# Performance work log

Measured on AMD Instinct MI355X. Metric: run time of the kernel, lower is better.

## Reference

```python
import jax, jax.numpy as jnp
import numpy as np

NEG = -1e8


def lstm_scan(x, lens, Wih, Whh, b):
    # x: [B,S,D], lens: [B] int. PyTorch gate order i,f,g,o. Returns [B,S,H], zero at pad.
    B, S, D = x.shape
    H = Whh.shape[1]
    xs = jnp.swapaxes(x, 0, 1)  # [S,B,D]
    ts = jnp.arange(S)

    def step(carry, inp):
        h, c = carry
        xt, t = inp
        gates = xt @ Wih.T + h @ Whh.T + b  # [B,4H]
        i, f, g, o = jnp.split(gates, 4, axis=-1)
        i, f, o = jax.nn.sigmoid(i), jax.nn.sigmoid(f), jax.nn.sigmoid(o)
        g = jnp.tanh(g)
        c_new = f * c + i * g
        h_new = o * jnp.tanh(c_new)
        valid = (t < lens)[:, None]
        h = jnp.where(valid, h_new, h)
        c = jnp.where(valid, c_new, c)
        out = jnp.where(valid, h_new, 0.0)
        return (h, c), out

    init = (jnp.zeros((B, H), x.dtype), jnp.zeros((B, H), x.dtype))
    _, outs = jax.lax.scan(step, init, (xs, ts))
    return jnp.swapaxes(outs, 0, 1)  # [B,S,H]


def bilstm(x, lens, Wih_f, Whh_f, b_f, Wih_b, Whh_b, b_b):
    # forward direction
    out_f = lstm_scan(x, lens, Wih_f, Whh_f, b_f)
    # backward: reverse the valid prefix per sample (packed-sequence semantics)
    S = x.shape[1]
    t = jnp.arange(S)[None, :]
    idx = jnp.where(t < lens[:, None], lens[:, None] - 1 - t, t)  # [B,S]
    xr = jnp.take_along_axis(x, idx[:, :, None], axis=1)
    out_r = lstm_scan(xr, lens, Wih_b, Whh_b, b_b)
    out_b = jnp.take_along_axis(out_r, idx[:, :, None], axis=1)
    return jnp.concatenate([out_f, out_b], axis=-1)


def tnet_forward(seqs_id, seqs_len, asps_len, asps_mask, sent_mask,
                 embed, Wih_f, Whh_f, b_f, Wih_b, Whh_b, b_b,
                 W_cpt, b_cpt, W_as, b_as, Wq, bq, Wk, bk, Wv, bv, Wd, bd):
    seqs = embed[seqs_id]                                   # [B,S,D] (dropout = eval identity)
    seqs_lstm = bilstm(seqs, seqs_len, Wih_f, Whh_f, b_f, Wih_b, Whh_b, b_b)  # [B,S,D]

    # ragged aspect gather + pad + mean == masked mean (asps_mask==0 marks aspect tokens)
    asp_sel = (asps_mask == 0).astype(seqs_lstm.dtype)       # [B,S]
    asps = (seqs_lstm * asp_sel[:, :, None]).sum(axis=1) / asps_len[:, None].astype(seqs_lstm.dtype)
    asps = asps[:, None, :]                                  # [B,1,D]

    # CPT layers (flag='AS'); Attentions = dot-product attn, out = softmax(QK^T + mask) @ K
    x = seqs_lstm
    for _ in range(2):
        score = jax.nn.softmax(jnp.einsum('bqd,bkd->bqk', x, seqs_lstm) + asps_mask[:, None, :], axis=-1)
        attn_out = jnp.einsum('bqk,bkd->bqd', score, seqs_lstm)
        combine = jnp.concatenate([attn_out, x], axis=-1)    # [B,S,2D]
        linear_out = jax.nn.relu(combine @ W_cpt.T + b_cpt)
        scale = jax.nn.sigmoid(x @ W_as.T + b_as)
        x = scale * linear_out + (1.0 - scale) * x

    # QKVAttention over sentence
    D = x.shape[-1]
    Qp = asps @ Wq.T + bq                                    # [B,1,D]
    Kp = x @ Wk.T + bk                                       # [B,S,D]
    Vp = x @ Wv.T + bv
    sc = jax.nn.softmax(jnp.einsum('bqd,bkd->bqk', Qp, Kp) / jnp.sqrt(jnp.asarray(D, x.dtype))
                        + sent_mask[:, None, :], axis=-1)    # [B,1,S]
    out = jnp.einsum('bqk,bkd->bqd', sc, Vp)                 # [B,1,D]
    logits = out[:, 0] @ Wd.T + bd                           # [B,n_class]
    return logits, sc[:, 0]


def setup_inputs() -> dict:
    B, S, V, D, H, NC = 64, 256, 30000, 512, 256, 3
    key = jax.random.key(0)
    ks = jax.random.split(key, 24)

    seqs_id = jax.random.randint(ks[0], (B, S), 0, V)
    seqs_len = jax.random.randint(ks[1], (B,), S // 2, S + 1)
    asps_len = jax.random.randint(ks[2], (B,), 1, 6)
    start = jax.random.randint(ks[3], (B,), 0, S // 2 - 8)   # aspect span inside valid prefix
    pos = jnp.arange(S)[None, :]
    in_span = (pos >= start[:, None]) & (pos < (start + asps_len)[:, None])
    asps_mask = jnp.where(in_span, 0.0, NEG).astype(jnp.float32)
    sent_mask = jnp.where(pos < seqs_len[:, None], 0.0, NEG).astype(jnp.float32)

    def nrm(k, shape, s=0.02):
        return (s * jax.random.normal(k, shape)).astype(jnp.float32)

    inp = dict(seqs_id=seqs_id, seqs_len=seqs_len, asps_len=asps_len,
               asps_mask=asps_mask, sent_mask=sent_mask,
               embed=nrm(ks[4], (V, D), 0.1),
               Wih_f=nrm(ks[5], (4 * H, D)), Whh_f=nrm(ks[6], (4 * H, H)), b_f=jnp.zeros((4 * H,), jnp.float32),
               Wih_b=nrm(ks[7], (4 * H, D)), Whh_b=nrm(ks[8], (4 * H, H)), b_b=jnp.zeros((4 * H,), jnp.float32),
               W_cpt=nrm(ks[9], (D, 2 * D)), b_cpt=jnp.zeros((D,), jnp.float32),
               W_as=nrm(ks[10], (D, D)), b_as=jnp.zeros((D,), jnp.float32),
               Wq=nrm(ks[11], (D, D)), bq=jnp.zeros((D,), jnp.float32),
               Wk=nrm(ks[12], (D, D)), bk=jnp.zeros((D,), jnp.float32),
               Wv=nrm(ks[13], (D, D)), bv=jnp.zeros((D,), jnp.float32),
               Wd=nrm(ks[14], (NC, D)), bd=jnp.zeros((NC,), jnp.float32))
    return inp


def reference(seqs_id, seqs_len, asps_len, asps_mask, sent_mask,
              embed, Wih_f, Whh_f, b_f, Wih_b, Whh_b, b_b,
              W_cpt, b_cpt, W_as, b_as, Wq, bq, Wk, bk, Wv, bv, Wd, bd):
    return tnet_forward(seqs_id, seqs_len, asps_len, asps_mask, sent_mask,
                        embed, Wih_f, Whh_f, b_f, Wih_b, Whh_b, b_b,
                        W_cpt, b_cpt, W_as, b_as, Wq, bq, Wk, bk, Wv, bv, Wd, bd)
```

## Files before the change

### kernel.cpp

```cpp
#include <hip/hip_runtime.h>
#include <math.h>

constexpr int B_ = 64, S_ = 256, D_ = 512, H_ = 256, NC_ = 3;
constexpr int BS = B_ * S_;
constexpr int G4 = 4 * H_;

typedef __attribute__((ext_vector_type(4))) float f32x4;
typedef __attribute__((ext_vector_type(8))) short s16x8;
typedef unsigned short u16;
typedef unsigned long long u64;

template<int ACT>
static __device__ __forceinline__ float activate(float v) {
  if constexpr (ACT == 1) return v > 0.f ? v : 0.f;
  else if constexpr (ACT == 2) return 1.f / (1.f + expf(-v));
  else return v;
}

static __device__ __forceinline__ u16 f2bf_rne(float f) {
  unsigned u = __float_as_uint(f);
  return (u16)((u + 0x7FFFu + ((u >> 16) & 1u)) >> 16);
}
static __device__ __forceinline__ float bf2f(u16 h) {
  return __uint_as_float(((unsigned)h) << 16);
}
static __device__ __forceinline__ void splitf(float f, u16& h, u16& l) {
  h = f2bf_rne(f);
  float r = f - bf2f(h);
  l = f2bf_rne(r);
}

__global__ __launch_bounds__(256) void split_w(
    const float* __restrict__ src, u16* __restrict__ h, u16* __restrict__ l, int n4)
{
  int i = blockIdx.x * 256 + threadIdx.x;
  if (i >= n4) return;
  float4 v = ((const float4*)src)[i];
  ushort4 hh, ll;
  splitf(v.x, hh.x, ll.x); splitf(v.y, hh.y, ll.y);
  splitf(v.z, hh.z, ll.z); splitf(v.w, hh.w, ll.w);
  ((ushort4*)h)[i] = hh;
  ((ushort4*)l)[i] = ll;
}

__global__ __launch_bounds__(256) void gather_split(
    const float* __restrict__ embed, const int* __restrict__ gidx,
    u16* __restrict__ h, u16* __restrict__ l)
{
  int i = blockIdx.x * 256 + threadIdx.x;
  if (i >= BS * D_ / 4) return;
  int r = i >> 7;
  int c = (i & 127) << 2;
  float4 v = *(const float4*)(embed + (size_t)gidx[r] * D_ + c);
  ushort4 hh, ll;
  splitf(v.x, hh.x, ll.x); splitf(v.y, hh.y, ll.y);
  splitf(v.z, hh.z, ll.z); splitf(v.w, hh.w, ll.w);
  ((ushort4*)h)[i] = hh;
  ((ushort4*)l)[i] = ll;
}

template<int ACT, bool BT, bool ADDC, bool ASPL, bool BSPL, bool OSPL, bool A2>
__global__ __launch_bounds__(256) void mgemm(
    const float* __restrict__ Af, const u16* __restrict__ Ah, const u16* __restrict__ Al,
    const u16* __restrict__ Ah2, const u16* __restrict__ Al2,
    const float* __restrict__ Bf, const u16* __restrict__ Bh, const u16* __restrict__ Bl,
    const float* __restrict__ bias, const float* __restrict__ Cin,
    float* __restrict__ Co, u16* __restrict__ Oh, u16* __restrict__ Ol,
    int M, int N, int K, int ldb, long sA, long sB, long sC, int ksp)
{
  __shared__ u16 AH[128][40];
  __shared__ u16 AL[128][40];
  __shared__ u16 BH[128][40];
  __shared__ u16 BL[128][40];

  const int tid = threadIdx.x;
  const int w = tid >> 6, l = tid & 63;
  const int m0 = blockIdx.x * 128, n0 = blockIdx.y * 128;
  const long zA = (long)blockIdx.z * sA;
  const long zB = (long)blockIdx.z * sB;
  const long zC = (long)blockIdx.z * sC;

  f32x4 acc[2][8];
  #pragma unroll
  for (int i = 0; i < 2; ++i)
    #pragma unroll
    for (int j = 0; j < 8; ++j) acc[i][j] = (f32x4){0.f, 0.f, 0.f, 0.f};

  const int ar = tid >> 1, ahh = tid & 1;
  const int bk = tid >> 3, bnq = tid & 7;
  const int lr = l & 15, lk = (l >> 4) * 8;

  for (int kt = 0; kt < K; kt += 32) {
    {
      int m = m0 + ar;
      if constexpr (ASPL) {
        const u16* srcH = Ah;
        const u16* srcL = Al;
        int kc = kt, kspan = K;
        if constexpr (A2) {
          if (kt >= ksp) { srcH = Ah2; srcL = Al2; kc = kt - ksp; }
          kspan = ksp;
        }
        s16x8 h0 = (s16x8)0, h1 = (s16x8)0, l0 = (s16x8)0, l1 = (s16x8)0;
        if (m < M) {
          const u16* ph = srcH + zA + (size_t)m * kspan + kc + ahh * 16;
          const u16* pl = srcL + zA + (size_t)m * kspan + kc + ahh * 16;
          h0 = *(const s16x8*)ph; h1 = *(const s16x8*)(ph + 8);
          l0 = *(const s16x8*)pl; l1 = *(const s16x8*)(pl + 8);
        }
        *(s16x8*)&AH[ar][ahh * 16] = h0; *(s16x8*)&AH[ar][ahh * 16 + 8] = h1;
        *(s16x8*)&AL[ar][ahh * 16] = l0; *(s16x8*)&AL[ar][ahh * 16 + 8] = l1;
      } else {
        float vv[16];
        if (m < M) {
          const float* pf = Af + zA + (size_t)m * K + kt + ahh * 16;
          #pragma unroll
          for (int c = 0; c < 4; ++c) {
            float4 v = ((const float4*)pf)[c];
            vv[c * 4] = v.x; vv[c * 4 + 1] = v.y; vv[c * 4 + 2] = v.z; vv[c * 4 + 3] = v.w;
          }
        } else {
          #pragma unroll
          for (int c = 0; c < 16; ++c) vv[c] = 0.f;
        }
        u16 hh[16], ll[16];
        #pragma unroll
        for (int c = 0; c < 16; ++c) splitf(vv[c], hh[c], ll[c]);
        *(s16x8*)&AH[ar][ahh * 16] = *(s16x8*)&hh[0];
        *(s16x8*)&AH[ar][ahh * 16 + 8] = *(s16x8*)&hh[8];
        *(s16x8*)&AL[ar][ahh * 16] = *(s16x8*)&ll[0];
        *(s16x8*)&AL[ar][ahh * 16 + 8] = *(s16x8*)&ll[8];
      }
    }
    if constexpr (BT) {
      if constexpr (BSPL) {
        const u16* ph = Bh + zB + (size_t)(n0 + ar) * ldb + kt + ahh * 16;
        const u16* pl = Bl + zB + (size_t)(n0 + ar) * ldb + kt + ahh * 16;
        *(s16x8*)&BH[ar][ahh * 16] = *(const s16x8*)ph;
        *(s16x8*)&BH[ar][ahh * 16 + 8] = *(const s16x8*)(ph + 8);
        *(s16x8*)&BL[ar][ahh * 16] = *(const s16x8*)pl;
        *(s16x8*)&BL[ar][ahh * 16 + 8] = *(const s16x8*)(pl + 8);
      } else {
        const float* pf = Bf + zB + (size_t)(n0 + ar) * ldb + kt + ahh * 16;
        float vv[16];
        #pragma unroll
        for (int c = 0; c < 4; ++c) {
          float4 v = ((const float4*)pf)[c];
          vv[c * 4] = v.x; vv[c * 4 + 1] = v.y; vv[c * 4 + 2] = v.z; vv[c * 4 + 3] = v.w;
        }
        u16 hh[16], ll[16];
        #pragma unroll
        for (int c = 0; c < 16; ++c) splitf(vv[c], hh[c], ll[c]);
        *(s16x8*)&BH[ar][ahh * 16] = *(s16x8*)&hh[0];
        *(s16x8*)&BH[ar][ahh * 16 + 8] = *(s16x8*)&hh[8];
        *(s16x8*)&BL[ar][ahh * 16] = *(s16x8*)&ll[0];
        *(s16x8*)&BL[ar][ahh * 16 + 8] = *(s16x8*)&ll[8];
      }
    } else {
      const u16* ph = Bh + zB + (size_t)(kt + bk) * ldb + n0 + bnq * 16;
      const u16* pl = Bl + zB + (size_t)(kt + bk) * ldb + n0 + bnq * 16;
      s16x8 h8a = *(const s16x8*)ph, h8b = *(const s16x8*)(ph + 8);
      s16x8 l8a = *(const s16x8*)pl, l8b = *(const s16x8*)(pl + 8);
      #pragma unroll
      for (int jj = 0; jj < 8; ++jj) {
        BH[bnq * 16 + jj][bk] = (u16)h8a[jj];
        BH[bnq * 16 + 8 + jj][bk] = (u16)h8b[jj];
        BL[bnq * 16 + jj][bk] = (u16)l8a[jj];
        BL[bnq * 16 + 8 + jj][bk] = (u16)l8b[jj];
      }
    }
    __syncthreads();

    s16x8 afh[2], afl[2];
    #pragma unroll
    for (int i = 0; i < 2; ++i) {
      afh[i] = *(const s16x8*)&AH[w * 32 + i * 16 + lr][lk];
      afl[i] = *(const s16x8*)&AL[w * 32 + i * 16 + lr][lk];
    }
    #pragma unroll
    for (int j = 0; j < 8; ++j) {
      s16x8 bfh = *(const s16x8*)&BH[j * 16 + lr][lk];
      s16x8 bfl = *(const s16x8*)&BL[j * 16 + lr][lk];
      #pragma unroll
      for (int i = 0; i < 2; ++i) {
        acc[i][j] = __builtin_amdgcn_mfma_f32_16x16x32_bf16(afl[i], bfh, acc[i][j], 0, 0, 0);
        acc[i][j] = __builtin_amdgcn_mfma_f32_16x16x32_bf16(afh[i], bfl, acc[i][j], 0, 0, 0);
        acc[i][j] = __builtin_amdgcn_mfma_f32_16x16x32_bf16(afh[i], bfh, acc[i][j], 0, 0, 0);
      }
    }
    __syncthreads();
  }

  const int rl = (l >> 4) * 4;
  #pragma unroll
  for (int j = 0; j < 8; ++j) {
    int n = n0 + j * 16 + lr;
    float bv = bias ? bias[n] : 0.f;
    #pragma unroll
    for (int i = 0; i < 2; ++i) {
      #pragma unroll
      for (int e = 0; e < 4; ++e) {
        int m = m0 + w * 32 + i * 16 + rl + e;
        if (m < M) {
          float v = acc[i][j][e] + bv;
          if constexpr (ADDC) v += Cin[zC + (size_t)m * N + n];
          v = activate<ACT>(v);
          if constexpr (OSPL) {
            u16 hh, ll; splitf(v, hh, ll);
            Oh[zC + (size_t)m * N + n] = hh;
            Ol[zC + (size_t)m * N + n] = ll;
          } else {
            Co[zC + (size_t)m * N + n] = v;
          }
        }
      }
    }
  }
}

__global__ __launch_bounds__(256) void wf_prep(
    const float* __restrict__ Wf, const float* __restrict__ Wb, u16* __restrict__ WF)
{
  int gid = blockIdx.x * 256 + threadIdx.x;
  int lane = gid & 63;
  int nt = (gid >> 6) & 1;
  int kt = (gid >> 7) & 7;
  int w  = (gid >> 10) & 3;
  int j  = (gid >> 12) & 7;
  int dir = gid >> 15;
  const float* W = dir ? Wb : Wf;
  int r = w * 256 + j * 32 + nt * 16 + (lane & 15);
  int kb = kt * 32 + (lane >> 4) * 8;
  const float* src = W + (size_t)r * H_ + kb;
  u16 hh[8], ll[8];
  #pragma unroll
  for (int c = 0; c < 2; ++c) {
    float4 v = ((const float4*)src)[c];
    splitf(v.x, hh[c*4+0], ll[c*4+0]); splitf(v.y, hh[c*4+1], ll[c*4+1]);
    splitf(v.z, hh[c*4+2], ll[c*4+2]); splitf(v.w, hh[c*4+3], ll[c*4+3]);
  }
  size_t off = (size_t)(gid >> 6) * 1024 + (size_t)lane * 8;
  *(s16x8*)(WF + off)       = *(s16x8*)&hh[0];
  *(s16x8*)(WF + off + 512) = *(s16x8*)&ll[0];
}

__global__ __launch_bounds__(256) void ring_init(u64* __restrict__ ring64)
{
  int i = blockIdx.x * 256 + threadIdx.x;
  __hip_atomic_store(&ring64[i], (u64)3, __ATOMIC_RELAXED, __HIP_MEMORY_SCOPE_AGENT);
}

__global__ __launch_bounds__(256, 1) void lstm_dist(
    const float* __restrict__ GX, const u16* __restrict__ WF,
    const int* __restrict__ lens, u16* __restrict__ outH, u16* __restrict__ outL,
    u64* __restrict__ ring64)
{
  const int bid = blockIdx.x;
  const int grp = bid & 7;
  const int j   = bid >> 3;
  const int dir = grp >> 2;
  const int bg  = grp & 3;
  const int b0g = bg * 16;
  const int tid = threadIdx.x;
  const int w = tid >> 6, l = tid & 63;

  const float* gx = GX + (size_t)dir * ((size_t)BS * G4);

  __shared__ int slen[16];
  __shared__ __align__(16) u16 AHs[16][264];
  __shared__ __align__(16) u16 ALs[16][264];
  __shared__ float act[2][4][16][33];
  if (tid < 16) slen[tid] = lens[b0g + tid];
  __syncthreads();

  s16x8 wh[8][2], wl[8][2];
  #pragma unroll
  for (int kt = 0; kt < 8; ++kt)
    #pragma unroll
    for (int nt = 0; nt < 2; ++nt) {
      size_t q = ((size_t)(((dir * 8 + j) * 4 + w) * 8 + kt) * 2 + nt);
      const u16* p = WF + q * 1024 + (size_t)l * 8;
      wh[kt][nt] = *(const s16x8*)p;
      wl[kt][nt] = *(const s16x8*)(p + 512);
    }

  const int ub = tid >> 4;
  const int uu = (tid & 15) * 2;
  const int len_b = slen[ub];
  float c0s = 0.f, c1s = 0.f, h0s = 0.f, h1s = 0.f;

  const int lr = l & 15, lkb = (l >> 4) * 8;

  for (int t = 0; t < S_; ++t) {
    float gxv[2][4];
    #pragma unroll
    for (int nt = 0; nt < 2; ++nt)
      #pragma unroll
      for (int e = 0; e < 4; ++e) {
        int b = (l >> 4) * 4 + e;
        int len = slen[b];
        int pos = dir ? (t < len ? len - 1 - t : t) : t;
        gxv[nt][e] = gx[(size_t)((b0g + b) * S_ + pos) * G4 + (w * 256 + j * 32 + nt * 16 + lr)];
      }

    f32x4 acc[2];
    acc[0] = (f32x4){0.f, 0.f, 0.f, 0.f};
    acc[1] = (f32x4){0.f, 0.f, 0.f, 0.f};

    if (t > 0) {
      const unsigned gen = (unsigned)(((t - 1) >> 2) & 3);
      const int slot = (t - 1) & 3;
      u64* rb = ring64 + ((size_t)slot * 8 + grp) * (16 * 128);
      u64 v[8];
      unsigned need = 0xFFu;
      do {
        unsigned nn = 0;
        #pragma unroll
        for (int k = 0; k < 8; ++k)
          if ((need >> k) & 1)
            v[k] = __hip_atomic_load(&rb[k * 256 + tid], __ATOMIC_RELAXED, __HIP_MEMORY_SCOPE_AGENT);
        #pragma unroll
        for (int k = 0; k < 8; ++k)
          if (((need >> k) & 1) && ((unsigned)v[k] & 3u) != gen) nn |= 1u << k;
        need = nn;
      } while (need);
      #pragma unroll
      for (int k = 0; k < 8; ++k) {
        int idx = k * 256 + tid;
        int b = idx >> 7, p = idx & 127;
        float f0 = __uint_as_float((unsigned)v[k] & ~3u);
        float f1 = __uint_as_float((unsigned)(v[k] >> 32));
        u16 hh0, ll0, hh1, ll1;
        splitf(f0, hh0, ll0); splitf(f1, hh1, ll1);
        *(unsigned*)&AHs[b][2 * p] = (unsigned)hh0 | ((unsigned)hh1 << 16);
        *(unsigned*)&ALs[b][2 * p] = (unsigned)ll0 | ((unsigned)ll1 << 16);
      }
      __syncthreads();
      #pragma unroll
      for (int kt = 0; kt < 8; ++kt) {
        s16x8 ah = *(const s16x8*)&AHs[lr][kt * 32 + lkb];
        s16x8 al = *(const s16x8*)&ALs[lr][kt * 32 + lkb];
        #pragma unroll
        for (int nt = 0; nt < 2; ++nt) {
          acc[nt] = __builtin_amdgcn_mfma_f32_16x16x32_bf16(al, wh[kt][nt], acc[nt], 0, 0, 0);
          acc[nt] = __builtin_amdgcn_mfma_f32_16x16x32_bf16(ah, wl[kt][nt], acc[nt], 0, 0, 0);
          acc[nt] = __builtin_amdgcn_mfma_f32_16x16x32_bf16(ah, wh[kt][nt], acc[nt], 0, 0, 0);
        }
      }
    }

    const int pb = t & 1;
    #pragma unroll
    for (int nt = 0; nt < 2; ++nt)
      #pragma unroll
      for (int e = 0; e < 4; ++e) {
        float v = acc[nt][e] + gxv[nt][e];
        v = (w == 2) ? tanhf(v) : 1.f / (1.f + expf(-v));
        act[pb][w][(l >> 4) * 4 + e][nt * 16 + lr] = v;
      }
    __syncthreads();

    {
      int pos = dir ? (t < len_b ? len_b - 1 - t : t) : t;
      bool valid = t < len_b;
      float i0 = act[pb][0][ub][uu],     f0 = act[pb][1][ub][uu],     g0 = act[pb][2][ub][uu],     o0 = act[pb][3][ub][uu];
      float i1 = act[pb][0][ub][uu + 1], f1 = act[pb][1][ub][uu + 1], g1 = act[pb][2][ub][uu + 1], o1 = act[pb][3][ub][uu + 1];
      float cn0 = fmaf(f0, c0s, i0 * g0), cn1 = fmaf(f1, c1s, i1 * g1);
      float hn0 = o0 * tanhf(cn0), hn1 = o1 * tanhf(cn1);
      if (valid) { c0s = cn0; h0s = hn0; c1s = cn1; h1s = hn1; }
      unsigned gen = (unsigned)((t >> 2) & 3);
      unsigned a0 = (__float_as_uint(h0s) & ~3u) | gen;
      unsigned a1 = __float_as_uint(h1s);
      u64 word = ((u64)a1 << 32) | (u64)a0;
      const int slot = t & 3;
      size_t ridx = ((size_t)slot * 8 + grp) * (16 * 128) + (size_t)ub * 128 + j * 16 + (tid & 15);
      __hip_atomic_store(&ring64[ridx], word, __ATOMIC_RELAXED, __HIP_MEMORY_SCOPE_AGENT);
      float ov0 = valid ? hn0 : 0.f, ov1 = valid ? hn1 : 0.f;
      u16 oh0, qq0, oh1, qq1;
      splitf(ov0, oh0, qq0); splitf(ov1, oh1, qq1);
      size_t obase = (size_t)((b0g + ub) * S_ + pos) * (2 * H_) + dir * H_ + j * 32 + uu;
      *(ushort2*)&outH[obase] = make_ushort2(oh0, oh1);
      *(ushort2*)&outL[obase] = make_ushort2(qq0, qq1);
    }
  }
}

__global__ __launch_bounds__(512) void asps_k(
    const u16* __restrict__ lh, const u16* __restrict__ ll,
    const float* __restrict__ amask, const int* __restrict__ alen, float* __restrict__ asps)
{
  int b = blockIdx.x, tid = threadIdx.x;
  __shared__ int sstart;
  if (tid == 0) sstart = S_;
  __syncthreads();
  if (tid < S_ && amask[b * S_ + tid] == 0.f) atomicMin(&sstart, tid);
  __syncthreads();
  const int start = sstart;
  const int len = alen[b];
  float acc = 0.f;
  for (int k = 0; k < len; ++k) {
    size_t i = ((size_t)(b * S_ + start + k)) * D_ + tid;
    acc += bf2f(lh[i]) + bf2f(ll[i]);
  }
  asps[b * D_ + tid] = acc / (float)len;
}

__global__ __launch_bounds__(256) void softmax_rows(
    const float* __restrict__ p_, const float* __restrict__ mask,
    u16* __restrict__ ph, u16* __restrict__ pl)
{
  const int row = blockIdx.x;
  const int b = row >> 8;
  const int tid = threadIdx.x;
  const float* p = p_ + (size_t)row * S_;
  float v = p[tid] + mask[(b << 8) | tid];
  float m = v;
  #pragma unroll
  for (int off = 32; off > 0; off >>= 1) m = fmaxf(m, __shfl_xor(m, off));
  __shared__ float r1[4];
  __shared__ float r2[4];
  const int w = tid >> 6, l = tid & 63;
  if (l == 0) r1[w] = m;
  __syncthreads();
  m = fmaxf(fmaxf(r1[0], r1[1]), fmaxf(r1[2], r1[3]));
  float e = expf(v - m);
  float s = e;
  #pragma unroll
  for (int off = 32; off > 0; off >>= 1) s += __shfl_xor(s, off);
  if (l == 0) r2[w] = s;
  __syncthreads();
  s = r2[0] + r2[1] + r2[2] + r2[3];
  float o = e / s;
  u16 hh, ll; splitf(o, hh, ll);
  ph[(size_t)row * S_ + tid] = hh;
  pl[(size_t)row * S_ + tid] = ll;
}

__global__ __launch_bounds__(256) void xupdate(
    const u16* __restrict__ xh, const u16* __restrict__ xl,
    const float4* __restrict__ sc, const float4* __restrict__ lin,
    u16* __restrict__ oh, u16* __restrict__ ol, int n4)
{
  int i = blockIdx.x * 256 + threadIdx.x;
  if (i >= n4) return;
  ushort4 h4 = ((const ushort4*)xh)[i];
  ushort4 l4 = ((const ushort4*)xl)[i];
  float4 s = sc[i], lv = lin[i];
  float x0 = bf2f(h4.x) + bf2f(l4.x);
  float x1 = bf2f(h4.y) + bf2f(l4.y);
  float x2 = bf2f(h4.z) + bf2f(l4.z);
  float x3 = bf2f(h4.w) + bf2f(l4.w);
  float o0 = s.x * lv.x + (1.f - s.x) * x0;
  float o1 = s.y * lv.y + (1.f - s.y) * x1;
  float o2 = s.z * lv.z + (1.f - s.z) * x2;
  float o3 = s.w * lv.w + (1.f - s.w) * x3;
  ushort4 hh, ll;
  splitf(o0, hh.x, ll.x); splitf(o1, hh.y, ll.y);
  splitf(o2, hh.z, ll.z); splitf(o3, hh.w, ll.w);
  ((ushort4*)oh)[i] = hh;
  ((ushort4*)ol)[i] = ll;
}

__global__ __launch_bounds__(256) void final_sc_k(
    const float* __restrict__ Qp, const float* __restrict__ Kp,
    const float* __restrict__ smask, float* __restrict__ outsc)
{
  int b = blockIdx.x, tid = threadIdx.x;
  __shared__ float q[D_];
  q[tid] = Qp[b * D_ + tid];
  q[tid + 256] = Qp[b * D_ + tid + 256];
  __syncthreads();
  const float4* kr = (const float4*)(Kp + ((size_t)(b * S_ + tid)) * D_);
  float acc = 0.f;
  #pragma unroll 4
  for (int d = 0; d < D_ / 4; ++d) {
    float4 kv = kr[d];
    acc += q[4 * d] * kv.x + q[4 * d + 1] * kv.y + q[4 * d + 2] * kv.z + q[4 * d + 3] * kv.w;
  }
  float v = acc / sqrtf((float)D_) + smask[b * S_ + tid];
  float m = v;
  #pragma unroll
  for (int off = 32; off > 0; off >>= 1) m = fmaxf(m, __shfl_xor(m, off));
  __shared__ float r1[4];
  __shared__ float r2[4];
  const int w = tid >> 6, l = tid & 63;
  if (l == 0) r1[w] = m;
  __syncthreads();
  m = fmaxf(fmaxf(r1[0], r1[1]), fmaxf(r1[2], r1[3]));
  float e = expf(v - m);
  float s = e;
  #pragma unroll
  for (int off = 32; off > 0; off >>= 1) s += __shfl_xor(s, off);
  if (l == 0) r2[w] = s;
  __syncthreads();
  s = r2[0] + r2[1] + r2[2] + r2[3];
  outsc[b * S_ + tid] = e / s;
}

__global__ __launch_bounds__(512) void zero_outv(float* __restrict__ p)
{
  p[blockIdx.x * 512 + threadIdx.x] = 0.f;
}

__global__ __launch_bounds__(512) void out_vec_k(
    const float* __restrict__ sc, const float* __restrict__ Vp, float* __restrict__ outv)
{
  int b = blockIdx.x, d = threadIdx.x;
  int k0 = blockIdx.y * 32;
  __shared__ float s[32];
  if (d < 32) s[d] = sc[b * S_ + k0 + d];
  __syncthreads();
  float acc = 0.f;
  #pragma unroll
  for (int k = 0; k < 32; ++k)
    acc = fmaf(s[k], Vp[((size_t)(b * S_ + k0 + k)) * D_ + d], acc);
  atomicAdd(&outv[b * D_ + d], acc);
}

__global__ __launch_bounds__(192) void logits_k(
    const float* __restrict__ outv, const float* __restrict__ Wd,
    const float* __restrict__ bd, float* __restrict__ out)
{
  int b = blockIdx.x;
  int c = threadIdx.x >> 6, l = threadIdx.x & 63;
  float acc = 0.f;
  for (int d = l; d < D_; d += 64) acc = fmaf(outv[b * D_ + d], Wd[c * D_ + d], acc);
  #pragma unroll
  for (int off = 32; off > 0; off >>= 1) acc += __shfl_down(acc, off);
  if (l == 0) out[b * NC_ + c] = acc + bd[c];
}

extern "C" void kernel_launch(void* const* d_in, const int* in_sizes, int n_in,
                              void* d_out, int out_size, void* d_ws, size_t ws_size,
                              hipStream_t stream)
{
  const int*   seqs_id   = (const int*)d_in[0];
  const int*   seqs_len  = (const int*)d_in[1];
  const int*   asps_len  = (const int*)d_in[2];
  const float* asps_mask = (const float*)d_in[3];
  const float* sent_mask = (const float*)d_in[4];
  const float* embed     = (const float*)d_in[5];
  const float* Wih_f     = (const float*)d_in[6];
  const float* Whh_f     = (const float*)d_in[7];
  const float* b_f       = (const float*)d_in[8];
  const float* Wih_b     = (const float*)d_in[9];
  const float* Whh_b     = (const float*)d_in[10];
  const float* b_b       = (const float*)d_in[11];
  const float* W_cpt     = (const float*)d_in[12];
  const float* b_cpt     = (const float*)d_in[13];
  const float* W_as      = (const float*)d_in[14];
  const float* b_as      = (const float*)d_in[15];
  const float* Wq        = (const float*)d_in[16];
  const float* bq        = (const float*)d_in[17];
  const float* Wk        = (const float*)d_in[18];
  const float* bk        = (const float*)d_in[19];
  const float* Wv        = (const float*)d_in[20];
  const float* bv        = (const float*)d_in[21];
  const float* Wd        = (const float*)d_in[22];
  const float* bd        = (const float*)d_in[23];

  float* w = (float*)d_ws;
  size_t off = 0;
  auto alloc = [&](size_t words) { size_t o = off; off += words; return o; };
  struct Split { u16* h; u16* l; };
  auto salloc = [&](size_t n) {
    size_t o = alloc(n);
    Split s; s.h = (u16*)(w + o); s.l = (u16*)(w + o) + n; return s;
  };

  const size_t off_wf   = alloc(524288);
  const size_t off_ring = alloc(131072);
  Split sWihF = salloc(4ul * H_ * D_);
  Split sWihB = salloc(4ul * H_ * D_);
  Split sWcpt = salloc((size_t)D_ * 2 * D_);
  Split sWas  = salloc((size_t)D_ * D_);
  Split sWk   = salloc((size_t)D_ * D_);
  Split sWv   = salloc((size_t)D_ * D_);
  Split sWq   = salloc((size_t)D_ * D_);
  Split sLstm = salloc((size_t)BS * D_);
  const size_t off_asps = alloc((size_t)B_ * D_);
  const size_t off_qp   = alloc((size_t)B_ * D_);
  const size_t off_outv = alloc((size_t)B_ * D_);

  const size_t dyn0 = off;
  Split sXemb; sXemb.h = (u16*)(w + dyn0); sXemb.l = sXemb.h + (size_t)BS * D_;
  float* GX = w + dyn0 + (size_t)BS * D_;
  size_t p2 = dyn0;
  float* scoreF = w + p2;                 p2 += (size_t)B_ * S_ * S_;
  Split sScore; sScore.h = (u16*)(w + p2); sScore.l = sScore.h + (size_t)B_ * S_ * S_; p2 += (size_t)B_ * S_ * S_;
  Split sAttn;  sAttn.h  = (u16*)(w + p2); sAttn.l  = sAttn.h + (size_t)BS * D_;       p2 += (size_t)BS * D_;
  float* lin = w + p2;                    p2 += (size_t)BS * D_;
  float* scl = w + p2;                    p2 += (size_t)BS * D_;
  Split sX;     sX.h     = (u16*)(w + p2); sX.l     = sX.h + (size_t)BS * D_;           p2 += (size_t)BS * D_;

  u16* WF      = (u16*)(w + off_wf);
  u64* ring64  = (u64*)(w + off_ring);
  float* aspsb = w + off_asps;
  float* qp    = w + off_qp;
  float* outv  = w + off_outv;
  float* Kp    = (float*)sAttn.h;
  float* Vp    = lin;
  float* logits = (float*)d_out;
  float* outsc  = (float*)d_out + B_ * NC_;

  ring_init<<<256, 256, 0, stream>>>(ring64);
  wf_prep<<<256, 256, 0, stream>>>(Whh_f, Whh_b, WF);
  split_w<<<512, 256, 0, stream>>>(Wih_f, sWihF.h, sWihF.l, H_ * D_);
  split_w<<<512, 256, 0, stream>>>(Wih_b, sWihB.h, sWihB.l, H_ * D_);
  split_w<<<512, 256, 0, stream>>>(W_cpt, sWcpt.h, sWcpt.l, D_ * 2 * D_ / 4);
  split_w<<<256, 256, 0, stream>>>(W_as, sWas.h, sWas.l, D_ * D_ / 4);
  split_w<<<256, 256, 0, stream>>>(Wk, sWk.h, sWk.l, D_ * D_ / 4);
  split_w<<<256, 256, 0, stream>>>(Wv, sWv.h, sWv.l, D_ * D_ / 4);
  split_w<<<256, 256, 0, stream>>>(Wq, sWq.h, sWq.l, D_ * D_ / 4);
  gather_split<<<BS * D_ / 4 / 256, 256, 0, stream>>>(embed, seqs_id, sXemb.h, sXemb.l);

  mgemm<0, true, false, true, true, false, false><<<dim3(128, 8, 1), 256, 0, stream>>>(
      nullptr, sXemb.h, sXemb.l, nullptr, nullptr, nullptr, sWihF.h, sWihF.l, b_f, nullptr,
      GX, nullptr, nullptr, BS, G4, D_, D_, 0, 0, 0, 0);
  mgemm<0, true, false, true, true, false, false><<<dim3(128, 8, 1), 256, 0, stream>>>(
      nullptr, sXemb.h, sXemb.l, nullptr, nullptr, nullptr, sWihB.h, sWihB.l, b_b, nullptr,
      GX + (size_t)BS * G4, nullptr, nullptr, BS, G4, D_, D_, 0, 0, 0, 0);

  lstm_dist<<<64, 256, 0, stream>>>(GX, WF, seqs_len, sLstm.h, sLstm.l, ring64);
  asps_k<<<B_, 512, 0, stream>>>(sLstm.h, sLstm.l, asps_mask, asps_len, aspsb);

  for (int it = 0; it < 2; ++it) {
    const Split xin = (it == 0) ? sLstm : sX;
    mgemm<0, true, false, true, true, false, false><<<dim3(2, 2, B_), 256, 0, stream>>>(
        nullptr, xin.h, xin.l, nullptr, nullptr, nullptr, sLstm.h, sLstm.l, nullptr, nullptr,
        scoreF, nullptr, nullptr, S_, S_, D_, D_,
        (long)S_ * D_, (long)S_ * D_, (long)S_ * S_, 0);
    softmax_rows<<<BS, 256, 0, stream>>>(scoreF, asps_mask, sScore.h, sScore.l);
    mgemm<0, false, false, true, true, true, false><<<dim3(2, 4, B_), 256, 0, stream>>>(
        nullptr, sScore.h, sScore.l, nullptr, nullptr, nullptr, sLstm.h, sLstm.l, nullptr, nullptr,
        nullptr, sAttn.h, sAttn.l, S_, D_, S_, D_,
        (long)S_ * S_, (long)S_ * D_, (long)S_ * D_, 0);
    mgemm<1, true, false, true, true, false, true><<<dim3(128, 4, 1), 256, 0, stream>>>(
        nullptr, sAttn.h, sAttn.l, xin.h, xin.l, nullptr, sWcpt.h, sWcpt.l, b_cpt, nullptr,
        lin, nullptr, nullptr, BS, D_, 2 * D_, 2 * D_, 0, 0, 0, D_);
    mgemm<2, true, false, true, true, false, false><<<dim3(128, 4, 1), 256, 0, stream>>>(
        nullptr, xin.h, xin.l, nullptr, nullptr, nullptr, sWas.h, sWas.l, b_as, nullptr,
        scl, nullptr, nullptr, BS, D_, D_, D_, 0, 0, 0, 0);
    xupdate<<<(BS * D_ / 4 + 255) / 256, 256, 0, stream>>>(
        xin.h, xin.l, (const float4*)scl, (const float4*)lin, sX.h, sX.l, BS * D_ / 4);
  }

  mgemm<0, true, false, true, true, false, false><<<dim3(128, 4, 1), 256, 0, stream>>>(
      nullptr, sX.h, sX.l, nullptr, nullptr, nullptr, sWk.h, sWk.l, bk, nullptr,
      Kp, nullptr, nullptr, BS, D_, D_, D_, 0, 0, 0, 0);
  mgemm<0, true, false, true, true, false, false><<<dim3(128, 4, 1), 256, 0, stream>>>(
      nullptr, sX.h, sX.l, nullptr, nullptr, nullptr, sWv.h, sWv.l, bv, nullptr,
      Vp, nullptr, nullptr, BS, D_, D_, D_, 0, 0, 0, 0);
  mgemm<0, true, false, false, true, false, false><<<dim3(1, 4, 1), 256, 0, stream>>>(
      aspsb, nullptr, nullptr, nullptr, nullptr, nullptr, sWq.h, sWq.l, bq, nullptr,
      qp, nullptr, nullptr, B_, D_, D_, D_, 0, 0, 0, 0);

  zero_outv<<<B_ * D_ / 512, 512, 0, stream>>>(outv);
  final_sc_k<<<B_, 256, 0, stream>>>(qp, Kp, sent_mask, outsc);
  out_vec_k<<<dim3(B_, 8, 1), 512, 0, stream>>>(outsc, Vp, outv);
  logits_k<<<B_, 192, 0, stream>>>(outv, Wd, bd, logits);
}
```

Before: 1.518 ms.

## Fuse score GEMM with masked softmax and fold gate update into GEMM epilogue

```diff
diff --git a/kernel.cpp b/kernel.cpp
--- a/kernel.cpp
+++ b/kernel.cpp
@@ -59,7 +59,7 @@
   ((ushort4*)l)[i] = ll;
 }
 
-template<int ACT, bool BT, bool ADDC, bool ASPL, bool BSPL, bool OSPL, bool A2>
+template<int ACT, bool BT, bool ADDC, bool ASPL, bool BSPL, bool OSPL, bool A2, bool XUP>
 __global__ __launch_bounds__(256) void mgemm(
     const float* __restrict__ Af, const u16* __restrict__ Ah, const u16* __restrict__ Al,
     const u16* __restrict__ Ah2, const u16* __restrict__ Al2,
@@ -205,7 +205,14 @@
           float v = acc[i][j][e] + bv;
           if constexpr (ADDC) v += Cin[zC + (size_t)m * N + n];
           v = activate<ACT>(v);
-          if constexpr (OSPL) {
+          if constexpr (XUP) {
+            float lv = Cin[zC + (size_t)m * N + n];
+            float xv = bf2f(Ah2[(size_t)m * N + n]) + bf2f(Al2[(size_t)m * N + n]);
+            float o = v * lv + (1.f - v) * xv;
+            u16 hh, ll; splitf(o, hh, ll);
+            Oh[zC + (size_t)m * N + n] = hh;
+            Ol[zC + (size_t)m * N + n] = ll;
+          } else if constexpr (OSPL) {
             u16 hh, ll; splitf(v, hh, ll);
             Oh[zC + (size_t)m * N + n] = hh;
             Ol[zC + (size_t)m * N + n] = ll;
@@ -213,6 +220,111 @@
             Co[zC + (size_t)m * N + n] = v;
           }
         }
+      }
+    }
+  }
+}
+
+__global__ __launch_bounds__(256) void score_sm(
+    const u16* __restrict__ Ah, const u16* __restrict__ Al,
+    const u16* __restrict__ Bh, const u16* __restrict__ Bl,
+    const float* __restrict__ mask,
+    u16* __restrict__ Oh, u16* __restrict__ Ol)
+{
+  __shared__ u16 AH[128][40];
+  __shared__ u16 AL[128][40];
+  __shared__ u16 BH[256][40];
+  __shared__ u16 BL[256][40];
+
+  const int tid = threadIdx.x;
+  const int w = tid >> 6, l = tid & 63;
+  const int m0 = blockIdx.x * 128;
+  const int z  = blockIdx.y;
+  const long zA = (long)z * (S_ * D_);
+  const long zC = (long)z * (S_ * S_);
+
+  f32x4 acc[2][16];
+  #pragma unroll
+  for (int i = 0; i < 2; ++i)
+    #pragma unroll
+    for (int j = 0; j < 16; ++j) acc[i][j] = (f32x4){0.f, 0.f, 0.f, 0.f};
+
+  const int ar = tid >> 1, ahh = tid & 1;
+  const int lr = l & 15, lk = (l >> 4) * 8;
+
+  for (int kt = 0; kt < D_; kt += 32) {
+    {
+      const u16* ph = Ah + zA + (size_t)(m0 + ar) * D_ + kt + ahh * 16;
+      const u16* pl = Al + zA + (size_t)(m0 + ar) * D_ + kt + ahh * 16;
+      *(s16x8*)&AH[ar][ahh * 16] = *(const s16x8*)ph;
+      *(s16x8*)&AH[ar][ahh * 16 + 8] = *(const s16x8*)(ph + 8);
+      *(s16x8*)&AL[ar][ahh * 16] = *(const s16x8*)pl;
+      *(s16x8*)&AL[ar][ahh * 16 + 8] = *(const s16x8*)(pl + 8);
+    }
+    #pragma unroll
+    for (int h = 0; h < 2; ++h) {
+      int r = h * 128 + ar;
+      const u16* ph = Bh + zA + (size_t)r * D_ + kt + ahh * 16;
+      const u16* pl = Bl + zA + (size_t)r * D_ + kt + ahh * 16;
+      *(s16x8*)&BH[r][ahh * 16] = *(const s16x8*)ph;
+      *(s16x8*)&BH[r][ahh * 16 + 8] = *(const s16x8*)(ph + 8);
+      *(s16x8*)&BL[r][ahh * 16] = *(const s16x8*)pl;
+      *(s16x8*)&BL[r][ahh * 16 + 8] = *(const s16x8*)(pl + 8);
+    }
+    __syncthreads();
+
+    s16x8 afh[2], afl[2];
+    #pragma unroll
+    for (int i = 0; i < 2; ++i) {
+      afh[i] = *(const s16x8*)&AH[w * 32 + i * 16 + lr][lk];
+      afl[i] = *(const s16x8*)&AL[w * 32 + i * 16 + lr][lk];
+    }
+    #pragma unroll
+    for (int j = 0; j < 16; ++j) {
+      s16x8 bfh = *(const s16x8*)&BH[j * 16 + lr][lk];
+      s16x8 bfl = *(const s16x8*)&BL[j * 16 + lr][lk];
+      #pragma unroll
+      for (int i = 0; i < 2; ++i) {
+        acc[i][j] = __builtin_amdgcn_mfma_f32_16x16x32_bf16(afl[i], bfh, acc[i][j], 0, 0, 0);
+        acc[i][j] = __builtin_amdgcn_mfma_f32_16x16x32_bf16(afh[i], bfl, acc[i][j], 0, 0, 0);
+        acc[i][j] = __builtin_amdgcn_mfma_f32_16x16x32_bf16(afh[i], bfh, acc[i][j], 0, 0, 0);
+      }
+    }
+    __syncthreads();
+  }
+
+  const int rl = (l >> 4) * 4;
+  float mk[16];
+  #pragma unroll
+  for (int j = 0; j < 16; ++j) mk[j] = mask[z * S_ + j * 16 + lr];
+
+  #pragma unroll
+  for (int i = 0; i < 2; ++i) {
+    #pragma unroll
+    for (int e = 0; e < 4; ++e) {
+      float val[16];
+      float vmax = -1e30f;
+      #pragma unroll
+      for (int j = 0; j < 16; ++j) {
+        val[j] = acc[i][j][e] + mk[j];
+        vmax = fmaxf(vmax, val[j]);
+      }
+      #pragma unroll
+      for (int off = 1; off < 16; off <<= 1)
+        vmax = fmaxf(vmax, __shfl_xor(vmax, off));
+      float sum = 0.f;
+      #pragma unroll
+      for (int j = 0; j < 16; ++j) { val[j] = expf(val[j] - vmax); sum += val[j]; }
+      #pragma unroll
+      for (int off = 1; off < 16; off <<= 1)
+        sum += __shfl_xor(sum, off);
+      float inv = 1.f / sum;
+      int r = m0 + w * 32 + i * 16 + rl + e;
+      #pragma unroll
+      for (int j = 0; j < 16; ++j) {
+        u16 hh, ll; splitf(val[j] * inv, hh, ll);
+        Oh[zC + (size_t)r * S_ + j * 16 + lr] = hh;
+        Ol[zC + (size_t)r * S_ + j * 16 + lr] = ll;
       }
     }
   }
@@ -403,62 +515,6 @@
     acc += bf2f(lh[i]) + bf2f(ll[i]);
   }
   asps[b * D_ + tid] = acc / (float)len;
-}
-
-__global__ __launch_bounds__(256) void softmax_rows(
-    const float* __restrict__ p_, const float* __restrict__ mask,
-    u16* __restrict__ ph, u16* __restrict__ pl)
-{
-  const int row = blockIdx.x;
-  const int b = row >> 8;
-  const int tid = threadIdx.x;
-  const float* p = p_ + (size_t)row * S_;
-  float v = p[tid] + mask[(b << 8) | tid];
-  float m = v;
-  #pragma unroll
-  for (int off = 32; off > 0; off >>= 1) m = fmaxf(m, __shfl_xor(m, off));
-  __shared__ float r1[4];
-  __shared__ float r2[4];
-  const int w = tid >> 6, l = tid & 63;
-  if (l == 0) r1[w] = m;
-  __syncthreads();
-  m = fmaxf(fmaxf(r1[0], r1[1]), fmaxf(r1[2], r1[3]));
-  float e = expf(v - m);
-  float s = e;
-  #pragma unroll
-  for (int off = 32; off > 0; off >>= 1) s += __shfl_xor(s, off);
-  if (l == 0) r2[w] = s;
-  __syncthreads();
-  s = r2[0] + r2[1] + r2[2] + r2[3];
-  float o = e / s;
-  u16 hh, ll; splitf(o, hh, ll);
-  ph[(size_t)row * S_ + tid] = hh;
-  pl[(size_t)row * S_ + tid] = ll;
-}
-
-__global__ __launch_bounds__(256) void xupdate(
-    const u16* __restrict__ xh, const u16* __restrict__ xl,
-    const float4* __restrict__ sc, const float4* __restrict__ lin,
-    u16* __restrict__ oh, u16* __restrict__ ol, int n4)
-{
-  int i = blockIdx.x * 256 + threadIdx.x;
-  if (i >= n4) return;
-  ushort4 h4 = ((const ushort4*)xh)[i];
-  ushort4 l4 = ((const ushort4*)xl)[i];
-  float4 s = sc[i], lv = lin[i];
-  float x0 = bf2f(h4.x) + bf2f(l4.x);
-  float x1 = bf2f(h4.y) + bf2f(l4.y);
-  float x2 = bf2f(h4.z) + bf2f(l4.z);
-  float x3 = bf2f(h4.w) + bf2f(l4.w);
-  float o0 = s.x * lv.x + (1.f - s.x) * x0;
-  float o1 = s.y * lv.y + (1.f - s.y) * x1;
-  float o2 = s.z * lv.z + (1.f - s.z) * x2;
-  float o3 = s.w * lv.w + (1.f - s.w) * x3;
-  ushort4 hh, ll;
-  splitf(o0, hh.x, ll.x); splitf(o1, hh.y, ll.y);
-  splitf(o2, hh.z, ll.z); splitf(o3, hh.w, ll.w);
-  ((ushort4*)oh)[i] = hh;
-  ((ushort4*)ol)[i] = ll;
 }
 
 __global__ __launch_bounds__(256) void final_sc_k(
@@ -586,7 +642,7 @@
   Split sXemb; sXemb.h = (u16*)(w + dyn0); sXemb.l = sXemb.h + (size_t)BS * D_;
   float* GX = w + dyn0 + (size_t)BS * D_;
   size_t p2 = dyn0;
-  float* scoreF = w + p2;                 p2 += (size_t)B_ * S_ * S_;
+  Split sX2;    sX2.h    = (u16*)(w + p2); sX2.l    = sX2.h + (size_t)BS * D_;         p2 += (size_t)B_ * S_ * S_;
   Split sScore; sScore.h = (u16*)(w + p2); sScore.l = sScore.h + (size_t)B_ * S_ * S_; p2 += (size_t)B_ * S_ * S_;
   Split sAttn;  sAttn.h  = (u16*)(w + p2); sAttn.l  = sAttn.h + (size_t)BS * D_;       p2 += (size_t)BS * D_;
   float* lin = w + p2;                    p2 += (size_t)BS * D_;
@@ -602,6 +658,7 @@
   float* Vp    = lin;
   float* logits = (float*)d_out;
   float* outsc  = (float*)d_out + B_ * NC_;
+  (void)scl;
 
   ring_init<<<256, 256, 0, stream>>>(ring64);
   wf_prep<<<256, 256, 0, stream>>>(Whh_f, Whh_b, WF);
@@ -614,10 +671,10 @@
   split_w<<<256, 256, 0, stream>>>(Wq, sWq.h, sWq.l, D_ * D_ / 4);
   gather_split<<<BS * D_ / 4 / 256, 256, 0, stream>>>(embed, seqs_id, sXemb.h, sXemb.l);
 
-  mgemm<0, true, false, true, true, false, false><<<dim3(128, 8, 1), 256, 0, stream>>>(
+  mgemm<0, true, false, true, true, false, false, false><<<dim3(128, 8, 1), 256, 0, stream>>>(
       nullptr, sXemb.h, sXemb.l, nullptr, nullptr, nullptr, sWihF.h, sWihF.l, b_f, nullptr,
       GX, nullptr, nullptr, BS, G4, D_, D_, 0, 0, 0, 0);
-  mgemm<0, true, false, true, true, false, false><<<dim3(128, 8, 1), 256, 0, stream>>>(
+  mgemm<0, true, false, true, true, false, false, false><<<dim3(128, 8, 1), 256, 0, stream>>>(
       nullptr, sXemb.h, sXemb.l, nullptr, nullptr, nullptr, sWihB.h, sWihB.l, b_b, nullptr,
       GX + (size_t)BS * G4, nullptr, nullptr, BS, G4, D_, D_, 0, 0, 0, 0);
 
@@ -625,33 +682,29 @@
   asps_k<<<B_, 512, 0, stream>>>(sLstm.h, sLstm.l, asps_mask, asps_len, aspsb);
 
   for (int it = 0; it < 2; ++it) {
-    const Split xin = (it == 0) ? sLstm : sX;
-    mgemm<0, true, false, true, true, false, false><<<dim3(2, 2, B_), 256, 0, stream>>>(
-        nullptr, xin.h, xin.l, nullptr, nullptr, nullptr, sLstm.h, sLstm.l, nullptr, nullptr,
-        scoreF, nullptr, nullptr, S_, S_, D_, D_,
-        (long)S_ * D_, (long)S_ * D_, (long)S_ * S_, 0);
-    softmax_rows<<<BS, 256, 0, stream>>>(scoreF, asps_mask, sScore.h, sScore.l);
-    mgemm<0, false, false, true, true, true, false><<<dim3(2, 4, B_), 256, 0, stream>>>(
+    const Split xin  = (it == 0) ? sLstm : sX;
+    const Split xout = (it == 0) ? sX    : sX2;
+    score_sm<<<dim3(2, B_), 256, 0, stream>>>(
+        xin.h, xin.l, sLstm.h, sLstm.l, asps_mask, sScore.h, sScore.l);
+    mgemm<0, false, false, true, true, true, false, false><<<dim3(2, 4, B_), 256, 0, stream>>>(
         nullptr, sScore.h, sScore.l, nullptr, nullptr, nullptr, sLstm.h, sLstm.l, nullptr, nullptr,
         nullptr, sAttn.h, sAttn.l, S_, D_, S_, D_,
         (long)S_ * S_, (long)S_ * D_, (long)S_ * D_, 0);
-    mgemm<1, true, false, true, true, false, true><<<dim3(128, 4, 1), 256, 0, stream>>>(
+    mgemm<1, true, false, true, true, false, true, false><<<dim3(128, 4, 1), 256, 0, stream>>>(
         nullptr, sAttn.h, sAttn.l, xin.h, xin.l, nullptr, sWcpt.h, sWcpt.l, b_cpt, nullptr,
         lin, nullptr, nullptr, BS, D_, 2 * D_, 2 * D_, 0, 0, 0, D_);
-    mgemm<2, true, false, true, true, false, false><<<dim3(128, 4, 1), 256, 0, stream>>>(
-        nullptr, xin.h, xin.l, nullptr, nullptr, nullptr, sWas.h, sWas.l, b_as, nullptr,
-        scl, nullptr, nullptr, BS, D_, D_, D_, 0, 0, 0, 0);
-    xupdate<<<(BS * D_ / 4 + 255) / 256, 256, 0, stream>>>(
-        xin.h, xin.l, (const float4*)scl, (const float4*)lin, sX.h, sX.l, BS * D_ / 4);
-  }
-
-  mgemm<0, true, false, true, true, false, false><<<dim3(128, 4, 1), 256, 0, stream>>>(
-      nullptr, sX.h, sX.l, nullptr, nullptr, nullptr, sWk.h, sWk.l, bk, nullptr,
+    mgemm<2, true, false, true, true, false, false, true><<<dim3(128, 4, 1), 256, 0, stream>>>(
+        nullptr, xin.h, xin.l, xin.h, xin.l, nullptr, sWas.h, sWas.l, b_as, lin,
+        nullptr, xout.h, xout.l, BS, D_, D_, D_, 0, 0, 0, 0);
+  }
+
+  mgemm<0, true, false, true, true, false, false, false><<<dim3(128, 4, 1), 256, 0, stream>>>(
+      nullptr, sX2.h, sX2.l, nullptr, nullptr, nullptr, sWk.h, sWk.l, bk, nullptr,
       Kp, nullptr, nullptr, BS, D_, D_, D_, 0, 0, 0, 0);
-  mgemm<0, true, false, true, true, false, false><<<dim3(128, 4, 1), 256, 0, stream>>>(
-      nullptr, sX.h, sX.l, nullptr, nullptr, nullptr, sWv.h, sWv.l, bv, nullptr,
+  mgemm<0, true, false, true, true, false, false, false><<<dim3(128, 4, 1), 256, 0, stream>>>(
+      nullptr, sX2.h, sX2.l, nullptr, nullptr, nullptr, sWv.h, sWv.l, bv, nullptr,
       Vp, nullptr, nullptr, BS, D_, D_, D_, 0, 0, 0, 0);
-  mgemm<0, true, false, false, true, false, false><<<dim3(1, 4, 1), 256, 0, stream>>>(
+  mgemm<0, true, false, false, true, false, false, false><<<dim3(1, 4, 1), 256, 0, stream>>>(
       aspsb, nullptr, nullptr, nullptr, nullptr, nullptr, sWq.h, sWq.l, bq, nullptr,
       qp, nullptr, nullptr, B_, D_, D_, D_, 0, 0, 0, 0);
 
```

Result: no change. 1.510 ms (median of 2 runs) (-0.5%).
